# Kernel optimization log

Hardware: AMD Instinct MI355X
Metric: run time of the kernel (lower is better)

## Reference

```python
import jax, jax.numpy as jnp
import numpy as np

N = 2048
E = 512
H = 8
DH = E // H
L = 2
MAX_DIST = 10
LOCAL_DIST = 2
NUM_COLORS = 16
NEG_INF = -1e9


def _layer_norm(x, scale, bias, eps=1e-5):
    mu = jnp.mean(x, axis=-1, keepdims=True)
    var = jnp.mean(jnp.square(x - mu), axis=-1, keepdims=True)
    return (x - mu) * jax.lax.rsqrt(var + eps) * scale + bias


def setup_inputs() -> dict:
    key = jax.random.key(0)
    ks = jax.random.split(key, 12)
    s = 0.05  # weight init scale for numerical sanity
    return {
        "D": jax.random.randint(ks[0], (N, N), 0, MAX_DIST + 2, dtype=jnp.int32),
        "x": jax.random.normal(ks[1], (1, N, E), dtype=jnp.float32),
        "dist_emb": jax.random.normal(ks[2], (MAX_DIST + 2, 8), dtype=jnp.float32) * s,
        "dist_proj_w": jax.random.normal(ks[3], (1, 8), dtype=jnp.float32) * s,
        "dist_proj_b": jnp.zeros((1,), jnp.float32),
        "ln1_scale": jnp.ones((L, E), jnp.float32),
        "ln1_bias": jnp.zeros((L, E), jnp.float32),
        "in_proj_w": jax.random.normal(ks[4], (L, 3 * E, E), dtype=jnp.float32) * s,
        "in_proj_b": jnp.zeros((L, 3 * E), jnp.float32),
        "out_w": jax.random.normal(ks[5], (L, E, E), dtype=jnp.float32) * s,
        "out_b": jnp.zeros((L, E), jnp.float32),
        "ln2_scale": jnp.ones((L, E), jnp.float32),
        "ln2_bias": jnp.zeros((L, E), jnp.float32),
        "ff1_w": jax.random.normal(ks[6], (L, 2 * E, E), dtype=jnp.float32) * s,
        "ff1_b": jnp.zeros((L, 2 * E), jnp.float32),
        "ff2_w": jax.random.normal(ks[7], (L, E, 2 * E), dtype=jnp.float32) * s,
        "ff2_b": jnp.zeros((L, E), jnp.float32),
        "color_w": jax.random.normal(ks[8], (NUM_COLORS, E), dtype=jnp.float32) * s,
        "color_b": jnp.zeros((NUM_COLORS,), jnp.float32),
    }


def reference(D, x, dist_emb, dist_proj_w, dist_proj_b,
              ln1_scale, ln1_bias, in_proj_w, in_proj_b, out_w, out_b,
              ln2_scale, ln2_bias, ff1_w, ff1_b, ff2_w, ff2_b,
              color_w, color_b):
    # Distance encoder: clamp -> embed -> project to scalar bias per (i, j)
    d_clamped = jnp.clip(D, 0, MAX_DIST + 1)                        # [N, N]
    emb = dist_emb[d_clamped]                                       # [N, N, 8]
    bias = jnp.einsum('nme,e->nm', emb, dist_proj_w[0]) + dist_proj_b[0]
    # Graph-local sparsity: real bias within local_dist, -inf elsewhere
    attn_mask = jnp.where(D <= LOCAL_DIST, bias, NEG_INF)           # [N, N]

    scale = 1.0 / jnp.sqrt(jnp.asarray(DH, x.dtype))
    for l in range(L):
        # --- pre-norm multihead self-attention ---
        xn = _layer_norm(x, ln1_scale[l], ln1_bias[l])              # [1, N, E]
        qkv = jnp.einsum('bne,fe->bnf', xn, in_proj_w[l]) + in_proj_b[l]
        q, k, v = jnp.split(qkv, 3, axis=-1)                        # each [1, N, E]
        q = q.reshape(1, N, H, DH)
        k = k.reshape(1, N, H, DH)
        v = v.reshape(1, N, H, DH)
        scores = jnp.einsum('bnhd,bmhd->bhnm', q, k) * scale        # [1, H, N, N]
        scores = scores + attn_mask[None, None, :, :]
        probs = jax.nn.softmax(scores, axis=-1)
        attn = jnp.einsum('bhnm,bmhd->bnhd', probs, v).reshape(1, N, E)
        attn = jnp.einsum('bne,fe->bnf', attn, out_w[l]) + out_b[l]
        x = x + attn                                                # dropout = identity (eval)
        # --- pre-norm feed-forward ---
        xf = _layer_norm(x, ln2_scale[l], ln2_bias[l])
        h = jax.nn.relu(jnp.einsum('bne,fe->bnf', xf, ff1_w[l]) + ff1_b[l])
        ff = jnp.einsum('bnf,ef->bne', h, ff2_w[l]) + ff2_b[l]
        x = x + ff

    logits = jnp.einsum('bne,ce->bnc', x, color_w) + color_b        # [1, N, C]
    return jax.nn.softmax(logits, axis=-1)[0]                       # [N, C]
```

## Files before the change

kernel.cpp:

```cpp
#include <hip/hip_runtime.h>
#include <cstddef>
#include <cstdint>

#define NN 2048
#define EE 512
#define HH 8
#define QKVF 1536
#define NSEG 8

typedef __attribute__((ext_vector_type(4))) float f32x4;
typedef __attribute__((ext_vector_type(8))) short s16x8;
typedef __attribute__((ext_vector_type(4))) short s16x4;

static __device__ __forceinline__ unsigned short f2bf(float x) {
  union { float f; unsigned int u; } c; c.f = x;
  unsigned int r = (c.u + 0x7FFFu + ((c.u >> 16) & 1u)) >> 16;
  return (unsigned short)r;
}

#define GLL16(gp, lp) __builtin_amdgcn_global_load_lds( \
    (const __attribute__((address_space(1))) void*)(gp), \
    (__attribute__((address_space(3))) void*)(lp), 16, 0, 0)

__global__ __launch_bounds__(256) void prep(
    const float* __restrict__ s0, const float* __restrict__ s1,
    const float* __restrict__ s2, const float* __restrict__ s3,
    unsigned short* __restrict__ d0, unsigned short* __restrict__ d1,
    unsigned short* __restrict__ d2, unsigned short* __restrict__ d3,
    const int* __restrict__ D, const float* __restrict__ demb,
    const float* __restrict__ dpw, const float* __restrict__ dpb,
    float* __restrict__ wpk4) {
  int b = blockIdx.x;
  if (b < 4096) {
    int j = b * 256 + threadIdx.x;
    const float* s; unsigned short* d;
    if (j < 393216) { s = s0; d = d0; }
    else {
      j -= 393216;
      if (j < 131072) { s = s1; d = d1; }
      else {
        j -= 131072;
        if (j < 262144) { s = s2; d = d2; }
        else { j -= 262144; s = s3; d = d3; }
      }
    }
    float4 v = ((const float4*)s)[j];
    s16x4 o;
    o[0] = (short)f2bf(v.x); o[1] = (short)f2bf(v.y);
    o[2] = (short)f2bf(v.z); o[3] = (short)f2bf(v.w);
    ((s16x4*)d)[j] = o;
  } else {
    int e = (b - 4096) * 256 + threadIdx.x;
    float ws0 = 0.f, ws1 = 0.f, ws2 = 0.f;
#pragma unroll
    for (int k = 0; k < 8; k++) {
      float pw = dpw[k];
      ws0 += demb[k] * pw; ws1 += demb[8 + k] * pw; ws2 += demb[16 + k] * pw;
    }
    float bb = dpb[0];
    float w0 = __expf(ws0 + bb), w1 = __expf(ws1 + bb), w2 = __expf(ws2 + bb);
    int row = e >> 9;
    int u = e & 511;
    int base = (u >> 4) * 64 + (u & 15);
    f32x4 wv;
#pragma unroll
    for (int i = 0; i < 4; i++) {
      int d = D[(size_t)row * NN + base + 16 * i];
      wv[i] = (d == 0) ? w0 : (d == 1) ? w1 : (d == 2) ? w2 : 0.f;
    }
    ((f32x4*)wpk4)[e] = wv;
  }
}

__global__ __launch_bounds__(256) void ln_kernel(const float* __restrict__ x,
    const float* __restrict__ scale, const float* __restrict__ bias,
    unsigned short* __restrict__ out) {
  int row = blockIdx.x;
  int t = threadIdx.x;
  const float* xr = x + (size_t)row * EE;
  float a = xr[t], b = xr[t + 256];
  float s = a + b, q = a * a + b * b;
#pragma unroll
  for (int m = 1; m < 64; m <<= 1) {
    s += __shfl_xor(s, m);
    q += __shfl_xor(q, m);
  }
  __shared__ float ps[4], pq[4];
  int w = t >> 6;
  if ((t & 63) == 0) { ps[w] = s; pq[w] = q; }
  __syncthreads();
  s = ps[0] + ps[1] + ps[2] + ps[3];
  q = pq[0] + pq[1] + pq[2] + pq[3];
  float mu = s * (1.f / EE);
  float var = q * (1.f / EE) - mu * mu;
  float r = rsqrtf(var + 1e-5f);
  unsigned short* orow = out + (size_t)row * EE;
  orow[t] = f2bf((a - mu) * r * scale[t] + bias[t]);
  orow[t + 256] = f2bf((b - mu) * r * scale[t + 256] + bias[t + 256]);
}

template <int RELU, int RES, int OBF>
__global__ __launch_bounds__(256) void gemm_bf(
    const unsigned short* __restrict__ A, const unsigned short* __restrict__ B,
    const float* __restrict__ bias, const float* __restrict__ R,
    void* __restrict__ Cout, int M, int F, int K) {
  __shared__ __attribute__((aligned(16))) unsigned short Al[2][64 * 64];
  __shared__ __attribute__((aligned(16))) unsigned short Bl[2][64 * 64];
  const int t = threadIdx.x;
  const int w = t >> 6, l = t & 63;
  const int fr = l & 15, fs = l >> 4;
  const int bm = blockIdx.y * 64, bf = blockIdx.x * 64;
  const int srow = l >> 3, slot = l & 7;
  const int nk = K >> 6;

  f32x4 acc[4];
  f32x4 zero = {0.f, 0.f, 0.f, 0.f};
#pragma unroll
  for (int j = 0; j < 4; j++) acc[j] = zero;

  auto stage = [&](int kt, int bsel) {
    int k0 = kt * 64;
#pragma unroll
    for (int rnd = 0; rnd < 2; rnd++) {
      int rowblk = w * 2 + rnd;
      int row = rowblk * 8 + srow;
      int koff = (slot * 8) ^ ((row & 7) * 8);
      GLL16(A + (size_t)(bm + row) * K + k0 + koff, &Al[bsel][rowblk * 512]);
      GLL16(B + (size_t)(bf + row) * K + k0 + koff, &Bl[bsel][rowblk * 512]);
    }
  };

  stage(0, 0);
  __syncthreads();
  for (int kt = 0; kt < nk; kt++) {
    const int cur = kt & 1;
    if (kt + 1 < nk) stage(kt + 1, cur ^ 1);
    s16x8 af[2], bg[4][2];
    const int arow = w * 16 + fr;
#pragma unroll
    for (int ks = 0; ks < 2; ks++)
      af[ks] = *(const s16x8*)&Al[cur][arow * 64 + ((ks * 32 + fs * 8) ^ ((arow & 7) * 8))];
#pragma unroll
    for (int ni = 0; ni < 4; ni++)
#pragma unroll
      for (int ks = 0; ks < 2; ks++) {
        int row = 16 * ni + fr;
        bg[ni][ks] = *(const s16x8*)&Bl[cur][row * 64 + ((ks * 32 + fs * 8) ^ ((row & 7) * 8))];
      }
#pragma unroll
    for (int ni = 0; ni < 4; ni++)
#pragma unroll
      for (int ks = 0; ks < 2; ks++)
        acc[ni] = __builtin_amdgcn_mfma_f32_16x16x32_bf16(af[ks], bg[ni][ks], acc[ni], 0, 0, 0);
    __syncthreads();
  }

#pragma unroll
  for (int ni = 0; ni < 4; ni++) {
    int gcol = bf + 16 * ni + fr;
    float bb = bias[gcol];
#pragma unroll
    for (int r = 0; r < 4; r++) {
      int grow = bm + w * 16 + fs * 4 + r;
      float v = acc[ni][r] + bb;
      if (RELU) v = fmaxf(v, 0.f);
      if (RES) v += R[(size_t)grow * F + gcol];
      if (OBF) ((unsigned short*)Cout)[(size_t)grow * F + gcol] = f2bf(v);
      else ((float*)Cout)[(size_t)grow * F + gcol] = v;
    }
  }
}

__global__ __launch_bounds__(256) void attn_mfma(
    const unsigned short* __restrict__ qkv, const float* __restrict__ wpk4,
    float* __restrict__ po, float* __restrict__ lpart) {
  __shared__ __attribute__((aligned(16))) unsigned short Kl[64 * 64];
  __shared__ __attribute__((aligned(16))) unsigned short Vt[66 * 64];
  __shared__ __attribute__((aligned(16))) unsigned short Pl[4][16 * 64];
  const int t = threadIdx.x;
  const int w = t >> 6, l = t & 63;
  const int fr = l & 15, fs = l >> 4;
  const int h = blockIdx.y;
  const int seg = blockIdx.z;
  const int qrow0 = blockIdx.x * 64 + w * 16;
  const int kvbase = seg * (NN / NSEG);
  const float C2 = 0.18033688011112042f;

  if (t < 64) Vt[64 * 64 + t] = 0x3F80;

  s16x8 qf[2];
#pragma unroll
  for (int ks = 0; ks < 2; ks++)
    qf[ks] = *(const s16x8*)&qkv[(size_t)(qrow0 + fr) * QKVF + h * 64 + ks * 32 + fs * 8];

  f32x4 o[4], o4;
  f32x4 zero = {0.f, 0.f, 0.f, 0.f};
#pragma unroll
  for (int i = 0; i < 4; i++) o[i] = zero;
  o4 = zero;

  const int krow = t >> 2, kc = (t & 3) * 16;
  const int vkv = (t & 15) * 4, vd = (t >> 4) * 4;
  const unsigned short* kbase = qkv + EE + h * 64;
  const unsigned short* vbase = qkv + 2 * EE + h * 64;
  s16x8 kreg[2];
  s16x4 vreg[4];
#pragma unroll
  for (int i = 0; i < 2; i++)
    kreg[i] = *(const s16x8*)&kbase[(size_t)(kvbase + krow) * QKVF + kc + i * 8];
#pragma unroll
  for (int i = 0; i < 4; i++)
    vreg[i] = *(const s16x4*)&vbase[(size_t)(kvbase + vkv + i) * QKVF + vd];

  for (int ch = 0; ch < NN / NSEG / 64; ch++) {
    __syncthreads();
#pragma unroll
    for (int i = 0; i < 2; i++)
      *(s16x8*)&Kl[krow * 64 + ((kc + i * 8) ^ ((krow & 7) * 8))] = kreg[i];
#pragma unroll
    for (int dj = 0; dj < 4; dj++) {
      int d = vd + dj;
      s16x4 pk;
      pk[0] = vreg[0][dj]; pk[1] = vreg[1][dj]; pk[2] = vreg[2][dj]; pk[3] = vreg[3][dj];
      *(s16x4*)&Vt[d * 64 + (vkv ^ ((d & 7) * 8))] = pk;
    }
    __syncthreads();
    if (ch + 1 < NN / NSEG / 64) {
      int kv0 = kvbase + (ch + 1) * 64;
#pragma unroll
      for (int i = 0; i < 2; i++)
        kreg[i] = *(const s16x8*)&kbase[(size_t)(kv0 + krow) * QKVF + kc + i * 8];
#pragma unroll
      for (int i = 0; i < 4; i++)
        vreg[i] = *(const s16x4*)&vbase[(size_t)(kv0 + vkv + i) * QKVF + vd];
    }
    int gc = kvbase / 64 + ch;

    f32x4 s[4];
#pragma unroll
    for (int ni = 0; ni < 4; ni++) s[ni] = zero;
    __builtin_amdgcn_s_setprio(1);
#pragma unroll
    for (int ni = 0; ni < 4; ni++) {
      int row = 16 * ni + fr;
#pragma unroll
      for (int ks = 0; ks < 2; ks++) {
        s16x8 kf = *(const s16x8*)&Kl[row * 64 + ((ks * 32 + fs * 8) ^ ((row & 7) * 8))];
        s[ni] = __builtin_amdgcn_mfma_f32_16x16x32_bf16(qf[ks], kf, s[ni], 0, 0, 0);
      }
    }
    __builtin_amdgcn_s_setprio(0);
#pragma unroll
    for (int r = 0; r < 4; r++) {
      int prow = fs * 4 + r;
      f32x4 wv = *(const f32x4*)&wpk4[((size_t)(qrow0 + prow) * 512 + gc * 16 + fr) * 4];
#pragma unroll
      for (int ni = 0; ni < 4; ni++) {
        union { float f; unsigned int u; } c;
        c.f = exp2f(s[ni][r] * C2) * wv[ni];
        Pl[w][prow * 64 + ((16 * ni + fr) ^ ((prow & 7) * 8))] =
            (unsigned short)(c.u >> 16);
      }
    }
    __builtin_amdgcn_s_setprio(1);
#pragma unroll
    for (int ks = 0; ks < 2; ks++) {
      s16x8 pa = *(const s16x8*)&Pl[w][fr * 64 + ((ks * 32 + fs * 8) ^ ((fr & 7) * 8))];
#pragma unroll
      for (int dn = 0; dn < 4; dn++) {
        int row = 16 * dn + fr;
        s16x8 vf = *(const s16x8*)&Vt[row * 64 + ((ks * 32 + fs * 8) ^ ((row & 7) * 8))];
        o[dn] = __builtin_amdgcn_mfma_f32_16x16x32_bf16(pa, vf, o[dn], 0, 0, 0);
      }
      s16x8 vf4 = *(const s16x8*)&Vt[(64 + fr) * 64 + ((ks * 32 + fs * 8) ^ ((fr & 7) * 8))];
      o4 = __builtin_amdgcn_mfma_f32_16x16x32_bf16(pa, vf4, o4, 0, 0, 0);
    }
    __builtin_amdgcn_s_setprio(0);
  }
#pragma unroll
  for (int r = 0; r < 4; r++) {
    int row = qrow0 + fs * 4 + r;
#pragma unroll
    for (int dn = 0; dn < 4; dn++)
      po[((size_t)seg * NN + row) * EE + h * 64 + 16 * dn + fr] = o[dn][r];
    if (fr == 0) lpart[((size_t)seg * NN + row) * 8 + h] = o4[r];
  }
}

__global__ __launch_bounds__(256) void attn_combine(const float* __restrict__ po,
    const float* __restrict__ lpart, unsigned short* __restrict__ attnb) {
  int id = blockIdx.x * 256 + threadIdx.x;
  int row = id >> 7;
  int col = (id & 127) * 4;
  int h = col >> 6;
  float4 o = {0.f, 0.f, 0.f, 0.f};
  float lsum = 0.f;
#pragma unroll
  for (int s = 0; s < NSEG; s++) {
    float4 p4 = *(const float4*)&po[((size_t)s * NN + row) * EE + col];
    o.x += p4.x; o.y += p4.y; o.z += p4.z; o.w += p4.w;
    lsum += lpart[((size_t)s * NN + row) * 8 + h];
  }
  float inv = 1.f / lsum;
  s16x4 ob;
  ob[0] = (short)f2bf(o.x * inv); ob[1] = (short)f2bf(o.y * inv);
  ob[2] = (short)f2bf(o.z * inv); ob[3] = (short)f2bf(o.w * inv);
  *(s16x4*)&attnb[(size_t)row * EE + col] = ob;
}

__global__ __launch_bounds__(256) void logits_kernel(const float* __restrict__ x,
    const float* __restrict__ cw, const float* __restrict__ cb,
    float* __restrict__ out) {
  int t = threadIdx.x;
  int wv = t >> 6, lane = t & 63;
  int row = blockIdx.x * 4 + wv;
  const float* xr = x + (size_t)row * EE;
  int c = lane >> 2, p = lane & 3;
  const float* w = cw + c * EE;
  float s = 0.f;
  for (int e = p * 128; e < p * 128 + 128; e++) s += xr[e] * w[e];
  s += __shfl_xor(s, 1);
  s += __shfl_xor(s, 2);
  __shared__ float lg[4][16];
  if (p == 0) lg[wv][c] = s + cb[c];
  __syncthreads();
  if (lane < 16) {
    float mx = -INFINITY;
#pragma unroll
    for (int k = 0; k < 16; k++) mx = fmaxf(mx, lg[wv][k]);
    float sum = 0.f;
#pragma unroll
    for (int k = 0; k < 16; k++) sum += __expf(lg[wv][k] - mx);
    out[(size_t)row * 16 + lane] = __expf(lg[wv][lane] - mx) / sum;
  }
}

extern "C" void kernel_launch(void* const* d_in, const int* in_sizes, int n_in,
                              void* d_out, int out_size, void* d_ws, size_t ws_size,
                              hipStream_t stream) {
  const int* D = (const int*)d_in[0];
  const float* x = (const float*)d_in[1];
  const float* demb = (const float*)d_in[2];
  const float* dpw = (const float*)d_in[3];
  const float* dpb = (const float*)d_in[4];
  const float* ln1s = (const float*)d_in[5];
  const float* ln1b = (const float*)d_in[6];
  const float* ipw = (const float*)d_in[7];
  const float* ipb = (const float*)d_in[8];
  const float* ow = (const float*)d_in[9];
  const float* ob = (const float*)d_in[10];
  const float* ln2s = (const float*)d_in[11];
  const float* ln2b = (const float*)d_in[12];
  const float* f1w = (const float*)d_in[13];
  const float* f1b = (const float*)d_in[14];
  const float* f2w = (const float*)d_in[15];
  const float* f2b = (const float*)d_in[16];
  const float* cw = (const float*)d_in[17];
  const float* cb = (const float*)d_in[18];

  char* base = (char*)d_ws;
  float* wpk4 = (float*)base;
  float* xbuf = (float*)(base + (16u << 20));
  unsigned short* qkv = (unsigned short*)(base + (20u << 20));
  unsigned short* xn = (unsigned short*)(base + (26u << 20));
  unsigned short* attnb = (unsigned short*)(base + (28u << 20));
  unsigned short* hbuf = (unsigned short*)(base + (30u << 20));
  unsigned short* ipw_bf = (unsigned short*)(base + (34u << 20));
  unsigned short* ow_bf = (unsigned short*)(base + (37u << 20));
  unsigned short* f1w_bf = (unsigned short*)(base + (38u << 20));
  unsigned short* f2w_bf = (unsigned short*)(base + (40u << 20));
  float* po = (float*)(base + (42u << 20));
  float* lpart = (float*)(base + (74u << 20));

  prep<<<8192, 256, 0, stream>>>(ipw, ow, f1w, f2w,
      ipw_bf, ow_bf, f1w_bf, f2w_bf, D, demb, dpw, dpb, wpk4);

  for (int l = 0; l < 2; l++) {
    const float* xin = (l == 0) ? x : xbuf;
    ln_kernel<<<NN, 256, 0, stream>>>(xin, ln1s + l * EE, ln1b + l * EE, xn);
    gemm_bf<0, 0, 1><<<dim3(24, 32), 256, 0, stream>>>(
        xn, ipw_bf + (size_t)l * 786432, ipb + l * 1536, nullptr, qkv, NN, 1536, 512);
    attn_mfma<<<dim3(32, HH, NSEG), 256, 0, stream>>>(qkv, wpk4, po, lpart);
    attn_combine<<<1024, 256, 0, stream>>>(po, lpart, attnb);
    gemm_bf<0, 1, 0><<<dim3(8, 32), 256, 0, stream>>>(
        attnb, ow_bf + (size_t)l * 262144, ob + l * EE, xin, xbuf, NN, 512, 512);
    ln_kernel<<<NN, 256, 0, stream>>>(xbuf, ln2s + l * EE, ln2b + l * EE, xn);
    gemm_bf<1, 0, 1><<<dim3(16, 32), 256, 0, stream>>>(
        xn, f1w_bf + (size_t)l * 524288, f1b + l * 1024, nullptr, hbuf, NN, 1024, 512);
    gemm_bf<0, 1, 0><<<dim3(8, 32), 256, 0, stream>>>(
        hbuf, f2w_bf + (size_t)l * 524288, f2b + l * EE, xbuf, xbuf, NN, 512, 1024);
  }
  logits_kernel<<<NN / 4, 256, 0, stream>>>(xbuf, cw, cb, (float*)d_out);
}
```

Before: 300.3 us.

## Fuse split-KV attention combine into attention kernel via last-block atomic counter

Removes the separate attn_combine launch. Each attention block bumps a per-(query tile, head) atomic counter, and the last of the NSEG segment blocks to finish sums the partial outputs and normalizers and writes the bf16 result. The mask weights are now stored in natural column order so D can be read with vector loads. Swapping the MFMA operands yields transposed scores, so P can be written as packed 4-element stores. Counters are zeroed in an extra prep block, which adds atomics and threadfences and leaves the reduction tail serialized on the last block.

```diff
diff --git a/kernel.cpp b/kernel.cpp
--- a/kernel.cpp
+++ b/kernel.cpp
@@ -11,6 +11,7 @@
 typedef __attribute__((ext_vector_type(4))) float f32x4;
 typedef __attribute__((ext_vector_type(8))) short s16x8;
 typedef __attribute__((ext_vector_type(4))) short s16x4;
+typedef __attribute__((ext_vector_type(4))) int i32x4;
 
 static __device__ __forceinline__ unsigned short f2bf(float x) {
   union { float f; unsigned int u; } c; c.f = x;
@@ -29,7 +30,7 @@
     unsigned short* __restrict__ d2, unsigned short* __restrict__ d3,
     const int* __restrict__ D, const float* __restrict__ demb,
     const float* __restrict__ dpw, const float* __restrict__ dpb,
-    float* __restrict__ wpk4) {
+    float* __restrict__ wpk4, int* __restrict__ cnt) {
   int b = blockIdx.x;
   if (b < 4096) {
     int j = b * 256 + threadIdx.x;
@@ -49,7 +50,7 @@
     o[0] = (short)f2bf(v.x); o[1] = (short)f2bf(v.y);
     o[2] = (short)f2bf(v.z); o[3] = (short)f2bf(v.w);
     ((s16x4*)d)[j] = o;
-  } else {
+  } else if (b < 8192) {
     int e = (b - 4096) * 256 + threadIdx.x;
     float ws0 = 0.f, ws1 = 0.f, ws2 = 0.f;
 #pragma unroll
@@ -59,16 +60,18 @@
     }
     float bb = dpb[0];
     float w0 = __expf(ws0 + bb), w1 = __expf(ws1 + bb), w2 = __expf(ws2 + bb);
-    int row = e >> 9;
-    int u = e & 511;
-    int base = (u >> 4) * 64 + (u & 15);
+    int row = e >> 9, kvq = e & 511;
+    i32x4 dd = *(const i32x4*)&D[(size_t)row * NN + kvq * 4];
     f32x4 wv;
 #pragma unroll
     for (int i = 0; i < 4; i++) {
-      int d = D[(size_t)row * NN + base + 16 * i];
+      int d = dd[i];
       wv[i] = (d == 0) ? w0 : (d == 1) ? w1 : (d == 2) ? w2 : 0.f;
     }
     ((f32x4*)wpk4)[e] = wv;
+  } else {
+    int t = threadIdx.x;
+    cnt[t] = 0; cnt[t + 256] = 0;
   }
 }
 
@@ -173,16 +176,17 @@
 
 __global__ __launch_bounds__(256) void attn_mfma(
     const unsigned short* __restrict__ qkv, const float* __restrict__ wpk4,
-    float* __restrict__ po, float* __restrict__ lpart) {
+    float* __restrict__ po, float* __restrict__ lpart,
+    unsigned short* __restrict__ attnb, int* __restrict__ cnt) {
   __shared__ __attribute__((aligned(16))) unsigned short Kl[64 * 64];
   __shared__ __attribute__((aligned(16))) unsigned short Vt[66 * 64];
   __shared__ __attribute__((aligned(16))) unsigned short Pl[4][16 * 64];
+  __shared__ int done_s;
   const int t = threadIdx.x;
   const int w = t >> 6, l = t & 63;
   const int fr = l & 15, fs = l >> 4;
-  const int h = blockIdx.y;
-  const int seg = blockIdx.z;
-  const int qrow0 = blockIdx.x * 64 + w * 16;
+  const int bx = blockIdx.x, h = blockIdx.y, seg = blockIdx.z;
+  const int qrow0 = bx * 64 + w * 16;
   const int kvbase = seg * (NN / NSEG);
   const float C2 = 0.18033688011112042f;
 
@@ -234,7 +238,6 @@
       for (int i = 0; i < 4; i++)
         vreg[i] = *(const s16x4*)&vbase[(size_t)(kv0 + vkv + i) * QKVF + vd];
     }
-    int gc = kvbase / 64 + ch;
 
     f32x4 s[4];
 #pragma unroll
@@ -246,21 +249,22 @@
 #pragma unroll
       for (int ks = 0; ks < 2; ks++) {
         s16x8 kf = *(const s16x8*)&Kl[row * 64 + ((ks * 32 + fs * 8) ^ ((row & 7) * 8))];
-        s[ni] = __builtin_amdgcn_mfma_f32_16x16x32_bf16(qf[ks], kf, s[ni], 0, 0, 0);
+        s[ni] = __builtin_amdgcn_mfma_f32_16x16x32_bf16(kf, qf[ks], s[ni], 0, 0, 0);
       }
     }
     __builtin_amdgcn_s_setprio(0);
 #pragma unroll
-    for (int r = 0; r < 4; r++) {
-      int prow = fs * 4 + r;
-      f32x4 wv = *(const f32x4*)&wpk4[((size_t)(qrow0 + prow) * 512 + gc * 16 + fr) * 4];
-#pragma unroll
-      for (int ni = 0; ni < 4; ni++) {
+    for (int ni = 0; ni < 4; ni++) {
+      f32x4 wv = ((const f32x4*)wpk4)[
+          (size_t)(qrow0 + fr) * 512 + ((kvbase + ch * 64 + 16 * ni) >> 2) + fs];
+      s16x4 pk;
+#pragma unroll
+      for (int r = 0; r < 4; r++) {
         union { float f; unsigned int u; } c;
-        c.f = exp2f(s[ni][r] * C2) * wv[ni];
-        Pl[w][prow * 64 + ((16 * ni + fr) ^ ((prow & 7) * 8))] =
-            (unsigned short)(c.u >> 16);
+        c.f = exp2f(s[ni][r] * C2) * wv[r];
+        pk[r] = (short)(c.u >> 16);
       }
+      *(s16x4*)&Pl[w][fr * 64 + ((16 * ni + fs * 4) ^ ((fr & 7) * 8))] = pk;
     }
     __builtin_amdgcn_s_setprio(1);
 #pragma unroll
@@ -285,27 +289,32 @@
       po[((size_t)seg * NN + row) * EE + h * 64 + 16 * dn + fr] = o[dn][r];
     if (fr == 0) lpart[((size_t)seg * NN + row) * 8 + h] = o4[r];
   }
-}
-
-__global__ __launch_bounds__(256) void attn_combine(const float* __restrict__ po,
-    const float* __restrict__ lpart, unsigned short* __restrict__ attnb) {
-  int id = blockIdx.x * 256 + threadIdx.x;
-  int row = id >> 7;
-  int col = (id & 127) * 4;
-  int h = col >> 6;
-  float4 o = {0.f, 0.f, 0.f, 0.f};
-  float lsum = 0.f;
-#pragma unroll
-  for (int s = 0; s < NSEG; s++) {
-    float4 p4 = *(const float4*)&po[((size_t)s * NN + row) * EE + col];
-    o.x += p4.x; o.y += p4.y; o.z += p4.z; o.w += p4.w;
-    lsum += lpart[((size_t)s * NN + row) * 8 + h];
-  }
-  float inv = 1.f / lsum;
-  s16x4 ob;
-  ob[0] = (short)f2bf(o.x * inv); ob[1] = (short)f2bf(o.y * inv);
-  ob[2] = (short)f2bf(o.z * inv); ob[3] = (short)f2bf(o.w * inv);
-  *(s16x4*)&attnb[(size_t)row * EE + col] = ob;
+
+  __threadfence();
+  __syncthreads();
+  if (t == 0) done_s = atomicAdd(&cnt[bx * 8 + h], 1);
+  __syncthreads();
+  if (done_s == NSEG - 1) {
+    __threadfence();
+    int rr = t >> 2;
+    int row = bx * 64 + rr;
+    int colb = h * 64 + (t & 3) * 16;
+    float lsum = 0.f;
+#pragma unroll
+    for (int sg = 0; sg < NSEG; sg++) lsum += lpart[((size_t)sg * NN + row) * 8 + h];
+    float inv = 1.f / lsum;
+#pragma unroll
+    for (int q4 = 0; q4 < 4; q4++) {
+      f32x4 a4 = zero;
+#pragma unroll
+      for (int sg = 0; sg < NSEG; sg++)
+        a4 += *(const f32x4*)&po[((size_t)sg * NN + row) * EE + colb + q4 * 4];
+      s16x4 ob;
+#pragma unroll
+      for (int j = 0; j < 4; j++) ob[j] = (short)f2bf(a4[j] * inv);
+      *(s16x4*)&attnb[(size_t)row * EE + colb + q4 * 4] = ob;
+    }
+  }
 }
 
 __global__ __launch_bounds__(256) void logits_kernel(const float* __restrict__ x,
@@ -371,17 +380,18 @@
   unsigned short* f2w_bf = (unsigned short*)(base + (40u << 20));
   float* po = (float*)(base + (42u << 20));
   float* lpart = (float*)(base + (74u << 20));
-
-  prep<<<8192, 256, 0, stream>>>(ipw, ow, f1w, f2w,
-      ipw_bf, ow_bf, f1w_bf, f2w_bf, D, demb, dpw, dpb, wpk4);
+  int* cnt = (int*)(base + (75u << 20));
+
+  prep<<<8193, 256, 0, stream>>>(ipw, ow, f1w, f2w,
+      ipw_bf, ow_bf, f1w_bf, f2w_bf, D, demb, dpw, dpb, wpk4, cnt);
 
   for (int l = 0; l < 2; l++) {
     const float* xin = (l == 0) ? x : xbuf;
     ln_kernel<<<NN, 256, 0, stream>>>(xin, ln1s + l * EE, ln1b + l * EE, xn);
     gemm_bf<0, 0, 1><<<dim3(24, 32), 256, 0, stream>>>(
         xn, ipw_bf + (size_t)l * 786432, ipb + l * 1536, nullptr, qkv, NN, 1536, 512);
-    attn_mfma<<<dim3(32, HH, NSEG), 256, 0, stream>>>(qkv, wpk4, po, lpart);
-    attn_combine<<<1024, 256, 0, stream>>>(po, lpart, attnb);
+    attn_mfma<<<dim3(32, HH, NSEG), 256, 0, stream>>>(
+        qkv, wpk4, po, lpart, attnb, cnt + l * 256);
     gemm_bf<0, 1, 0><<<dim3(8, 32), 256, 0, stream>>>(
         attnb, ow_bf + (size_t)l * 262144, ob + l * EE, xin, xbuf, NN, 512, 512);
     ln_kernel<<<NN, 256, 0, stream>>>(xbuf, ln2s + l * EE, ln2b + l * EE, xn);
```

New measurement: 885.7 us. 195% more time.
